# Kernel optimization log

Measured on AMD Instinct MI355X. Metric: run time of the kernel, lower is better.

The kernel has to match this reference:

```python
import jax, jax.numpy as jnp
import numpy as np

B, H, S, D = 1, 16, 4096, 64

def setup_inputs() -> dict:
    key = jax.random.key(0)
    k1, k2, k3 = jax.random.split(key, 3)
    query = jax.random.normal(k1, (B, H, S, D), dtype=jnp.float32)
    key_t = jax.random.normal(k2, (B, H, S, D), dtype=jnp.float32)
    value = jax.random.normal(k3, (B, H, S, D), dtype=jnp.float32)
    attn_mask = jnp.zeros((B, 1, S, S), dtype=jnp.float32)
    return {"query": query, "key": key_t, "value": value, "attn_mask": attn_mask}

def reference(query, key, value, attn_mask):
    d = query.shape[-1]
    # [B,H,S,S] = QK^T / sqrt(d) + mask
    scores = jnp.einsum("bhqd,bhkd->bhqk", query, key) / jnp.sqrt(jnp.float32(d))
    scores = scores + attn_mask
    probs = jax.nn.softmax(scores, axis=-1)
    # dropout_p = 0.0 -> identity
    out = jnp.einsum("bhqk,bhkd->bhqd", probs, value)
    return out
```

## Files before the change

kernel.cpp:

```cpp
#include <hip/hip_runtime.h>
#include <stdint.h>

#define LOG2E  1.44269504088896f
#define QSCALE (0.125f * LOG2E)

typedef float    f32x4_t  __attribute__((ext_vector_type(4)));
typedef float    f32x16_t __attribute__((ext_vector_type(16)));
typedef _Float16 f16x8_t  __attribute__((ext_vector_type(8)));
typedef _Float16 f16x2_t  __attribute__((ext_vector_type(2)));

#if __has_builtin(__builtin_amdgcn_exp2f)
#define EXP2F(x) __builtin_amdgcn_exp2f(x)
#else
#define EXP2F(x) exp2f(x)
#endif

__device__ __forceinline__ float rowsum2(f16x2_t p, float acc) {
#if __has_builtin(__builtin_amdgcn_fdot2)
  return __builtin_amdgcn_fdot2(p, (f16x2_t){(_Float16)1.0f, (_Float16)1.0f}, acc, false);
#else
  return acc + (float)p[0] + (float)p[1];
#endif
}

__global__ void prep_kernel(const float* __restrict__ M, const float* __restrict__ K,
                            const float* __restrict__ V, _Float16* __restrict__ Kh,
                            _Float16* __restrict__ Vth, int* __restrict__ flag) {
  __shared__ __align__(16) _Float16 T[64 * 72];
  const int tid = threadIdx.x;
  const int bid = blockIdx.x;

  {
    const float* p = M + (size_t)bid * 8192 + (size_t)tid * 4;
    unsigned acc = 0;
#pragma unroll
    for (int i = 0; i < 8; ++i) {
      f32x4_t v = *(const f32x4_t*)(p + (size_t)i * 1024);
      acc |= __float_as_uint(v[0]) | __float_as_uint(v[1]) |
             __float_as_uint(v[2]) | __float_as_uint(v[3]);
    }
    if (acc & 0x7fffffffu) atomicOr(flag, 1);
  }

  if (Kh != nullptr) {
    {
      const size_t idx = ((size_t)bid * 256 + tid) * 8;
      f32x4_t a = *(const f32x4_t*)(K + idx);
      f32x4_t b = *(const f32x4_t*)(K + idx + 4);
      union { _Float16 h[8]; uint4 q; } U;
#pragma unroll
      for (int j = 0; j < 4; ++j) { U.h[j] = (_Float16)a[j]; U.h[4 + j] = (_Float16)b[j]; }
      *(uint4*)(Kh + idx) = U.q;
    }
    if (bid < 1024) {
      const int head = bid >> 6;
      const int st   = bid & 63;
      const size_t hoff = (size_t)head * 4096 * 64;
      const int sl    = tid >> 2;
      const int fbase = (tid & 3) * 16;
      const float* src = V + hoff + (size_t)(st * 64 + sl) * 64 + fbase;
#pragma unroll
      for (int c = 0; c < 4; ++c) {
        f32x4_t a = *(const f32x4_t*)(src + c * 4);
#pragma unroll
        for (int j = 0; j < 4; ++j) T[(fbase + c * 4 + j) * 72 + sl] = (_Float16)a[j];
      }
      __syncthreads();
      const int feat = tid >> 2;
      const int sb   = (tid & 3) * 16;
      uint4 r0 = *(const uint4*)&T[feat * 72 + sb];
      uint4 r1 = *(const uint4*)&T[feat * 72 + sb + 8];
      _Float16* dst = Vth + hoff + (size_t)feat * 4096 + st * 64 + sb;
      *(uint4*)(dst)     = r0;
      *(uint4*)(dst + 8) = r1;
    }
  }
}

template <bool WS16, int NS>
__launch_bounds__(256, (NS == 1) ? 2 : 4)
__global__ void sdpa_kernel(const float* __restrict__ Qg, const float* __restrict__ Kg,
                            const float* __restrict__ Vg, const float* __restrict__ Mg,
                            const _Float16* __restrict__ Kh, const _Float16* __restrict__ Vth,
                            float* __restrict__ Og, float* __restrict__ Opart,
                            float* __restrict__ Lpart, const int* __restrict__ flag) {
  __shared__ __align__(16) _Float16 Ks[64 * 72];
  __shared__ __align__(16) _Float16 Vt[64 * 72];

  constexpr int QTSH = (NS == 1) ? 4 : (NS == 2) ? 5 : 6;

  const int tid  = threadIdx.x;
  const int bid  = blockIdx.x;
  const int hh   = ((bid & 7) << 1) | ((bid >> 3) & 1);
  const int part = (NS == 1) ? 0 : ((bid >> 4) & (NS - 1));
  const int qt   = bid >> QTSH;
  const int w    = tid >> 6;
  const int lane = tid & 63;
  const int n    = lane & 31;
  const int h2   = lane >> 5;
  const int sig  = (n & 0x13) | ((n >> 1) & 4) | ((n << 1) & 8);
  const bool has_mask = (*flag) != 0;

  const size_t hoff = (size_t)hh * 4096 * 64;
  const int qcol = qt * 128 + w * 32 + n;
  const int ktn  = 64 / NS;
  const int ktlo = part * ktn;

  f16x8_t qf[4];
  {
    const float* qp = Qg + hoff + (size_t)qcol * 64 + 8 * h2;
#pragma unroll
    for (int kh = 0; kh < 4; ++kh) {
      f32x4_t a = *(const f32x4_t*)(qp + kh * 16);
      f32x4_t b = *(const f32x4_t*)(qp + kh * 16 + 4);
      union { _Float16 h[8]; f16x8_t v; } U;
#pragma unroll
      for (int j = 0; j < 4; ++j) { U.h[j] = (_Float16)(a[j] * QSCALE); U.h[4 + j] = (_Float16)(b[j] * QSCALE); }
      qf[kh] = U.v;
    }
  }

  f32x16_t o0 = {0.f,0.f,0.f,0.f,0.f,0.f,0.f,0.f,0.f,0.f,0.f,0.f,0.f,0.f,0.f,0.f};
  f32x16_t o1 = o0;
  float lacc = 0.0f;

#pragma unroll 1
  for (int kk = 0; kk < ktn; ++kk) {
    const int kt    = ktlo + kk;
    const int kbase = kt * 64;

    uint4 kk0, kk1, vv0, vv1;
    f32x4_t k0, k1, k2, k3;
    float vlo[8], vhi[8];
    if (WS16) {
      const _Float16* kp = Kh + hoff + (size_t)(kbase + (tid >> 2)) * 64 + (tid & 3) * 16;
      kk0 = *(const uint4*)(kp);
      kk1 = *(const uint4*)(kp + 8);
      const _Float16* vp = Vth + hoff + (size_t)(tid >> 2) * 4096 + kbase + (tid & 3) * 16;
      vv0 = *(const uint4*)(vp);
      vv1 = *(const uint4*)(vp + 8);
    } else {
      const float* kp = Kg + hoff + (size_t)(kbase + (tid >> 2)) * 64 + (tid & 3) * 16;
      k0 = *(const f32x4_t*)(kp + 0);
      k1 = *(const f32x4_t*)(kp + 4);
      k2 = *(const f32x4_t*)(kp + 8);
      k3 = *(const f32x4_t*)(kp + 12);
      const float* vp = Vg + hoff + (size_t)(kbase + (tid >> 5) * 8) * 64 + (tid & 31);
#pragma unroll
      for (int j = 0; j < 8; ++j) {
        vlo[j] = vp[(size_t)j * 64];
        vhi[j] = vp[(size_t)j * 64 + 32];
      }
    }

    f32x4_t mk[2][2][2];
    if (has_mask) {
      const float* mp = Mg + (size_t)qcol * 4096 + kbase + 8 * h2;
#pragma unroll
      for (int kb = 0; kb < 2; ++kb)
#pragma unroll
        for (int a = 0; a < 2; ++a)
#pragma unroll
          for (int b = 0; b < 2; ++b)
            mk[kb][a][b] = *(const f32x4_t*)(mp + kb * 32 + 16 * a + 4 * b);
    }

    __syncthreads();

    if (WS16) {
      *(uint4*)&Ks[(tid >> 2) * 72 + (tid & 3) * 16]     = kk0;
      *(uint4*)&Ks[(tid >> 2) * 72 + (tid & 3) * 16 + 8] = kk1;
      *(uint4*)&Vt[(tid >> 2) * 72 + (tid & 3) * 16]     = vv0;
      *(uint4*)&Vt[(tid >> 2) * 72 + (tid & 3) * 16 + 8] = vv1;
    } else {
      union { _Float16 h[8]; uint4 q; } A, B;
#pragma unroll
      for (int j = 0; j < 4; ++j) {
        A.h[j] = (_Float16)k0[j];  A.h[4 + j] = (_Float16)k1[j];
        B.h[j] = (_Float16)k2[j];  B.h[4 + j] = (_Float16)k3[j];
      }
      *(uint4*)&Ks[(tid >> 2) * 72 + (tid & 3) * 16]     = A.q;
      *(uint4*)&Ks[(tid >> 2) * 72 + (tid & 3) * 16 + 8] = B.q;
      union { _Float16 h[8]; uint4 q; } C, D;
#pragma unroll
      for (int j = 0; j < 8; ++j) { C.h[j] = (_Float16)vlo[j]; D.h[j] = (_Float16)vhi[j]; }
      *(uint4*)&Vt[(tid & 31) * 72 + (tid >> 5) * 8]        = C.q;
      *(uint4*)&Vt[((tid & 31) + 32) * 72 + (tid >> 5) * 8] = D.q;
    }

    __syncthreads();

#pragma unroll
    for (int kb = 0; kb < 2; ++kb) {
      f32x16_t acc = {0.f,0.f,0.f,0.f,0.f,0.f,0.f,0.f,0.f,0.f,0.f,0.f,0.f,0.f,0.f,0.f};
#pragma unroll
      for (int kh = 0; kh < 4; ++kh) {
        const f16x8_t ka = *(const f16x8_t*)&Ks[(kb * 32 + sig) * 72 + kh * 16 + 8 * h2];
        acc = __builtin_amdgcn_mfma_f32_32x32x16_f16(ka, qf[kh], acc, 0, 0, 0);
      }
#pragma unroll
      for (int a = 0; a < 2; ++a) {
        union { _Float16 h[8]; f16x8_t v; f16x2_t p2[4]; } F;
#pragma unroll
        for (int idx = 0; idx < 8; ++idx) {
          float x = acc[8 * a + idx];
          if (has_mask) x = __builtin_fmaf(mk[kb][a][idx >> 2][idx & 3], LOG2E, x);
          F.h[idx] = (_Float16)EXP2F(x);
        }
#pragma unroll
        for (int t = 0; t < 4; ++t) lacc = rowsum2(F.p2[t], lacc);
        const int f = kb * 2 + a;
        const f16x8_t v0 = *(const f16x8_t*)&Vt[n * 72 + f * 16 + 8 * h2];
        o0 = __builtin_amdgcn_mfma_f32_32x32x16_f16(F.v, v0, o0, 0, 0, 0);
        const f16x8_t v1 = *(const f16x8_t*)&Vt[(32 + n) * 72 + f * 16 + 8 * h2];
        o1 = __builtin_amdgcn_mfma_f32_32x32x16_f16(F.v, v1, o1, 0, 0, 0);
      }
    }
  }

  float lq = lacc + __shfl_xor(lacc, 32);
  if constexpr (NS > 1) {
    float* op = Opart + (size_t)part * (16 * 4096 * 64) + hoff;
#pragma unroll
    for (int r2 = 0; r2 < 4; ++r2) {
#pragma unroll
      for (int rr = 0; rr < 4; ++rr) {
        const int reg  = r2 * 4 + rr;
        const int qrow = rr + 8 * r2 + 4 * h2;
        const size_t row = (size_t)(qt * 128 + w * 32 + qrow) * 64;
        op[row + n]      = o0[reg];
        op[row + 32 + n] = o1[reg];
      }
    }
    if (h2 == 0)
      Lpart[(size_t)part * 65536 + (size_t)hh * 4096 + qcol] = lq;
  } else {
    float* op = Og + hoff;
#pragma unroll
    for (int r2 = 0; r2 < 4; ++r2) {
#pragma unroll
      for (int rr = 0; rr < 4; ++rr) {
        const int reg  = r2 * 4 + rr;
        const int qrow = rr + 8 * r2 + 4 * h2;
        float lr  = __shfl(lq, qrow);
        float inv = 1.0f / lr;
        const size_t row = (size_t)(qt * 128 + w * 32 + qrow) * 64;
        op[row + n]      = o0[reg] * inv;
        op[row + 32 + n] = o1[reg] * inv;
      }
    }
  }
}

template <int NS>
__global__ void combine_kernel(const float* __restrict__ Opart, const float* __restrict__ Lpart,
                               float* __restrict__ Og) {
  const size_t NELEM = (size_t)16 * 4096 * 64;
  const size_t e   = ((size_t)blockIdx.x * 256 + threadIdx.x) * 8;
  const size_t row = e >> 6;
  float lsum = 0.0f;
#pragma unroll
  for (int p = 0; p < NS; ++p) lsum += Lpart[(size_t)p * 65536 + row];
  const float inv = 1.0f / lsum;
  f32x4_t s0 = {0.f, 0.f, 0.f, 0.f}, s1 = s0;
#pragma unroll
  for (int p = 0; p < NS; ++p) {
    const float* a = Opart + (size_t)p * NELEM + e;
    f32x4_t x0 = *(const f32x4_t*)a;
    f32x4_t x1 = *(const f32x4_t*)(a + 4);
#pragma unroll
    for (int j = 0; j < 4; ++j) { s0[j] += x0[j]; s1[j] += x1[j]; }
  }
  f32x4_t r0, r1;
#pragma unroll
  for (int j = 0; j < 4; ++j) { r0[j] = s0[j] * inv; r1[j] = s1[j] * inv; }
  *(f32x4_t*)(Og + e)     = r0;
  *(f32x4_t*)(Og + e + 4) = r1;
}

extern "C" void kernel_launch(void* const* d_in, const int* in_sizes, int n_in,
                              void* d_out, int out_size, void* d_ws, size_t ws_size,
                              hipStream_t stream) {
  const float* Q = (const float*)d_in[0];
  const float* K = (const float*)d_in[1];
  const float* V = (const float*)d_in[2];
  const float* M = (const float*)d_in[3];
  float* O = (float*)d_out;

  const size_t NELEM = (size_t)16 * 4096 * 64;
  const size_t need16 = 256 + 2 * NELEM * sizeof(_Float16);
  const size_t need2  = need16 + 2 * NELEM * sizeof(float) + 2 * 65536 * sizeof(float);
  const size_t need4  = need16 + 4 * NELEM * sizeof(float) + 4 * 65536 * sizeof(float);
  int* flag = (int*)d_ws;
  const bool ws16 = (ws_size >= need16);
  _Float16* Kh    = ws16 ? (_Float16*)((char*)d_ws + 256) : nullptr;
  _Float16* Vth   = ws16 ? Kh + NELEM : nullptr;
  float*    Opart = ws16 ? (float*)(Vth + NELEM) : nullptr;
  float*    Lpart4 = ws16 ? Opart + 4 * NELEM : nullptr;
  float*    Lpart2 = ws16 ? Opart + 2 * NELEM : nullptr;

  hipMemsetAsync(flag, 0, sizeof(int), stream);
  prep_kernel<<<2048, 256, 0, stream>>>(M, K, V, Kh, Vth, flag);

  if (ws_size >= need4) {
    sdpa_kernel<true, 4><<<2048, 256, 0, stream>>>(Q, K, V, M, Kh, Vth, O, Opart, Lpart4, flag);
    combine_kernel<4><<<2048, 256, 0, stream>>>(Opart, Lpart4, O);
  } else if (ws_size >= need2) {
    sdpa_kernel<true, 2><<<1024, 256, 0, stream>>>(Q, K, V, M, Kh, Vth, O, Opart, Lpart2, flag);
    combine_kernel<2><<<2048, 256, 0, stream>>>(Opart, Lpart2, O);
  } else if (ws16) {
    sdpa_kernel<true, 1><<<512, 256, 0, stream>>>(Q, K, V, M, Kh, Vth, O, nullptr, nullptr, flag);
  } else {
    sdpa_kernel<false, 1><<<512, 256, 0, stream>>>(Q, K, V, M, nullptr, nullptr, O, nullptr, nullptr, flag);
  }
}
```

Measured before the change: 241.8 us.

## Prelayout K/V in MFMA fragment order and load operands directly from global

The prep kernel now writes fp16 K and V in an order that matches the MFMA operand fragments for each 64-key tile. The attention kernel then reads each lane's K and V operands straight from global memory or L2. This removes the per-tile LDS staging, both __syncthreads barriers and the shared memory, and allows higher occupancy (launch bounds 4 for every NS). The cost is that each wave now loads its own copy of the K/V tile, so four waves fetch the same data through the cache, and global load latency is no longer hidden by the cooperative staging.

```diff
diff --git a/kernel.cpp b/kernel.cpp
--- a/kernel.cpp
+++ b/kernel.cpp
@@ -23,9 +23,13 @@
 #endif
 }
 
+__device__ __forceinline__ int sigf(int n) {
+  return (n & 0x13) | ((n >> 1) & 4) | ((n << 1) & 8);
+}
+
 __global__ void prep_kernel(const float* __restrict__ M, const float* __restrict__ K,
-                            const float* __restrict__ V, _Float16* __restrict__ Kh,
-                            _Float16* __restrict__ Vth, int* __restrict__ flag) {
+                            const float* __restrict__ V, _Float16* __restrict__ Kf,
+                            _Float16* __restrict__ Vf, int* __restrict__ flag) {
   __shared__ __align__(16) _Float16 T[64 * 72];
   const int tid = threadIdx.x;
   const int bid = blockIdx.x;
@@ -42,15 +46,25 @@
     if (acc & 0x7fffffffu) atomicOr(flag, 1);
   }
 
-  if (Kh != nullptr) {
+  if (Kf != nullptr) {
     {
-      const size_t idx = ((size_t)bid * 256 + tid) * 8;
-      f32x4_t a = *(const f32x4_t*)(K + idx);
-      f32x4_t b = *(const f32x4_t*)(K + idx + 4);
+      const size_t flat8 = ((size_t)bid * 256 + tid) * 8;
+      const int head = (int)(flat8 >> 18);
+      const int rem  = (int)(flat8 & 0x3FFFF);
+      const int key  = rem >> 6;
+      const int o    = (rem >> 3) & 7;
+      const int kt   = key >> 6;
+      const int kb   = (key >> 5) & 1;
+      const int nn   = sigf(key & 31);
+      const int kh   = o >> 1;
+      const int h2o  = o & 1;
+      f32x4_t a = *(const f32x4_t*)(K + flat8);
+      f32x4_t b = *(const f32x4_t*)(K + flat8 + 4);
       union { _Float16 h[8]; uint4 q; } U;
 #pragma unroll
       for (int j = 0; j < 4; ++j) { U.h[j] = (_Float16)a[j]; U.h[4 + j] = (_Float16)b[j]; }
-      *(uint4*)(Kh + idx) = U.q;
+      const size_t chunk = (size_t)(head * 64 + kt) * 512 + (size_t)((kb * 8 + kh * 2 + h2o) * 32 + nn);
+      *(uint4*)(Kf + chunk * 8) = U.q;
     }
     if (bid < 1024) {
       const int head = bid >> 6;
@@ -66,27 +80,26 @@
         for (int j = 0; j < 4; ++j) T[(fbase + c * 4 + j) * 72 + sl] = (_Float16)a[j];
       }
       __syncthreads();
-      const int feat = tid >> 2;
-      const int sb   = (tid & 3) * 16;
-      uint4 r0 = *(const uint4*)&T[feat * 72 + sb];
-      uint4 r1 = *(const uint4*)&T[feat * 72 + sb + 8];
-      _Float16* dst = Vth + hoff + (size_t)feat * 4096 + st * 64 + sb;
-      *(uint4*)(dst)     = r0;
-      *(uint4*)(dst + 8) = r1;
-    }
-  }
-}
-
-template <bool WS16, int NS>
-__launch_bounds__(256, (NS == 1) ? 2 : 4)
-__global__ void sdpa_kernel(const float* __restrict__ Qg, const float* __restrict__ Kg,
-                            const float* __restrict__ Vg, const float* __restrict__ Mg,
-                            const _Float16* __restrict__ Kh, const _Float16* __restrict__ Vth,
+      const int f  = tid >> 6;
+      const int l  = tid & 63;
+      const int nn = l & 31;
+      const int hl = l >> 5;
+      const size_t tbase = (size_t)(head * 64 + st) * 512;
+#pragma unroll
+      for (int vh = 0; vh < 2; ++vh) {
+        uint4 r = *(const uint4*)&T[(nn + 32 * vh) * 72 + f * 16 + 8 * hl];
+        *(uint4*)(Vf + (tbase + (size_t)((f * 2 + vh) * 64 + l)) * 8) = r;
+      }
+    }
+  }
+}
+
+template <int NS>
+__launch_bounds__(256, 4)
+__global__ void sdpa_direct(const float* __restrict__ Qg, const float* __restrict__ Mg,
+                            const _Float16* __restrict__ Kf, const _Float16* __restrict__ Vf,
                             float* __restrict__ Og, float* __restrict__ Opart,
                             float* __restrict__ Lpart, const int* __restrict__ flag) {
-  __shared__ __align__(16) _Float16 Ks[64 * 72];
-  __shared__ __align__(16) _Float16 Vt[64 * 72];
-
   constexpr int QTSH = (NS == 1) ? 4 : (NS == 2) ? 5 : 6;
 
   const int tid  = threadIdx.x;
@@ -98,7 +111,6 @@
   const int lane = tid & 63;
   const int n    = lane & 31;
   const int h2   = lane >> 5;
-  const int sig  = (n & 0x13) | ((n >> 1) & 4) | ((n << 1) & 8);
   const bool has_mask = (*flag) != 0;
 
   const size_t hoff = (size_t)hh * 4096 * 64;
@@ -124,34 +136,12 @@
   f32x16_t o1 = o0;
   float lacc = 0.0f;
 
+  const _Float16* ktile = Kf + (size_t)(hh * 64 + ktlo) * 4096 + h2 * 256 + n * 8;
+  const _Float16* vtile = Vf + (size_t)(hh * 64 + ktlo) * 4096 + (size_t)lane * 8;
+
 #pragma unroll 1
   for (int kk = 0; kk < ktn; ++kk) {
-    const int kt    = ktlo + kk;
-    const int kbase = kt * 64;
-
-    uint4 kk0, kk1, vv0, vv1;
-    f32x4_t k0, k1, k2, k3;
-    float vlo[8], vhi[8];
-    if (WS16) {
-      const _Float16* kp = Kh + hoff + (size_t)(kbase + (tid >> 2)) * 64 + (tid & 3) * 16;
-      kk0 = *(const uint4*)(kp);
-      kk1 = *(const uint4*)(kp + 8);
-      const _Float16* vp = Vth + hoff + (size_t)(tid >> 2) * 4096 + kbase + (tid & 3) * 16;
-      vv0 = *(const uint4*)(vp);
-      vv1 = *(const uint4*)(vp + 8);
-    } else {
-      const float* kp = Kg + hoff + (size_t)(kbase + (tid >> 2)) * 64 + (tid & 3) * 16;
-      k0 = *(const f32x4_t*)(kp + 0);
-      k1 = *(const f32x4_t*)(kp + 4);
-      k2 = *(const f32x4_t*)(kp + 8);
-      k3 = *(const f32x4_t*)(kp + 12);
-      const float* vp = Vg + hoff + (size_t)(kbase + (tid >> 5) * 8) * 64 + (tid & 31);
-#pragma unroll
-      for (int j = 0; j < 8; ++j) {
-        vlo[j] = vp[(size_t)j * 64];
-        vhi[j] = vp[(size_t)j * 64 + 32];
-      }
-    }
+    const int kbase = (ktlo + kk) * 64;
 
     f32x4_t mk[2][2][2];
     if (has_mask) {
@@ -165,37 +155,12 @@
             mk[kb][a][b] = *(const f32x4_t*)(mp + kb * 32 + 16 * a + 4 * b);
     }
 
-    __syncthreads();
-
-    if (WS16) {
-      *(uint4*)&Ks[(tid >> 2) * 72 + (tid & 3) * 16]     = kk0;
-      *(uint4*)&Ks[(tid >> 2) * 72 + (tid & 3) * 16 + 8] = kk1;
-      *(uint4*)&Vt[(tid >> 2) * 72 + (tid & 3) * 16]     = vv0;
-      *(uint4*)&Vt[(tid >> 2) * 72 + (tid & 3) * 16 + 8] = vv1;
-    } else {
-      union { _Float16 h[8]; uint4 q; } A, B;
-#pragma unroll
-      for (int j = 0; j < 4; ++j) {
-        A.h[j] = (_Float16)k0[j];  A.h[4 + j] = (_Float16)k1[j];
-        B.h[j] = (_Float16)k2[j];  B.h[4 + j] = (_Float16)k3[j];
-      }
-      *(uint4*)&Ks[(tid >> 2) * 72 + (tid & 3) * 16]     = A.q;
-      *(uint4*)&Ks[(tid >> 2) * 72 + (tid & 3) * 16 + 8] = B.q;
-      union { _Float16 h[8]; uint4 q; } C, D;
-#pragma unroll
-      for (int j = 0; j < 8; ++j) { C.h[j] = (_Float16)vlo[j]; D.h[j] = (_Float16)vhi[j]; }
-      *(uint4*)&Vt[(tid & 31) * 72 + (tid >> 5) * 8]        = C.q;
-      *(uint4*)&Vt[((tid & 31) + 32) * 72 + (tid >> 5) * 8] = D.q;
-    }
-
-    __syncthreads();
-
 #pragma unroll
     for (int kb = 0; kb < 2; ++kb) {
       f32x16_t acc = {0.f,0.f,0.f,0.f,0.f,0.f,0.f,0.f,0.f,0.f,0.f,0.f,0.f,0.f,0.f,0.f};
 #pragma unroll
       for (int kh = 0; kh < 4; ++kh) {
-        const f16x8_t ka = *(const f16x8_t*)&Ks[(kb * 32 + sig) * 72 + kh * 16 + 8 * h2];
+        const f16x8_t ka = *(const f16x8_t*)(ktile + kb * 2048 + kh * 512);
         acc = __builtin_amdgcn_mfma_f32_32x32x16_f16(ka, qf[kh], acc, 0, 0, 0);
       }
 #pragma unroll
@@ -210,12 +175,14 @@
 #pragma unroll
         for (int t = 0; t < 4; ++t) lacc = rowsum2(F.p2[t], lacc);
         const int f = kb * 2 + a;
-        const f16x8_t v0 = *(const f16x8_t*)&Vt[n * 72 + f * 16 + 8 * h2];
+        const f16x8_t v0 = *(const f16x8_t*)(vtile + f * 1024);
         o0 = __builtin_amdgcn_mfma_f32_32x32x16_f16(F.v, v0, o0, 0, 0, 0);
-        const f16x8_t v1 = *(const f16x8_t*)&Vt[(32 + n) * 72 + f * 16 + 8 * h2];
+        const f16x8_t v1 = *(const f16x8_t*)(vtile + f * 1024 + 512);
         o1 = __builtin_amdgcn_mfma_f32_32x32x16_f16(F.v, v1, o1, 0, 0, 0);
       }
     }
+    ktile += 4096;
+    vtile += 4096;
   }
 
   float lq = lacc + __shfl_xor(lacc, 32);
@@ -252,6 +219,138 @@
   }
 }
 
+__launch_bounds__(256, 2)
+__global__ void sdpa_lds_fallback(const float* __restrict__ Qg, const float* __restrict__ Kg,
+                                  const float* __restrict__ Vg, const float* __restrict__ Mg,
+                                  float* __restrict__ Og, const int* __restrict__ flag) {
+  __shared__ __align__(16) _Float16 Ks[64 * 72];
+  __shared__ __align__(16) _Float16 Vt[64 * 72];
+
+  const int tid  = threadIdx.x;
+  const int bid  = blockIdx.x;
+  const int hh   = ((bid & 7) << 1) | ((bid >> 3) & 1);
+  const int qt   = bid >> 4;
+  const int w    = tid >> 6;
+  const int lane = tid & 63;
+  const int n    = lane & 31;
+  const int h2   = lane >> 5;
+  const int sig  = sigf(n);
+  const bool has_mask = (*flag) != 0;
+
+  const size_t hoff = (size_t)hh * 4096 * 64;
+  const int qcol = qt * 128 + w * 32 + n;
+
+  f16x8_t qf[4];
+  {
+    const float* qp = Qg + hoff + (size_t)qcol * 64 + 8 * h2;
+#pragma unroll
+    for (int kh = 0; kh < 4; ++kh) {
+      f32x4_t a = *(const f32x4_t*)(qp + kh * 16);
+      f32x4_t b = *(const f32x4_t*)(qp + kh * 16 + 4);
+      union { _Float16 h[8]; f16x8_t v; } U;
+#pragma unroll
+      for (int j = 0; j < 4; ++j) { U.h[j] = (_Float16)(a[j] * QSCALE); U.h[4 + j] = (_Float16)(b[j] * QSCALE); }
+      qf[kh] = U.v;
+    }
+  }
+
+  f32x16_t o0 = {0.f,0.f,0.f,0.f,0.f,0.f,0.f,0.f,0.f,0.f,0.f,0.f,0.f,0.f,0.f,0.f};
+  f32x16_t o1 = o0;
+  float lacc = 0.0f;
+
+#pragma unroll 1
+  for (int kt = 0; kt < 64; ++kt) {
+    const int kbase = kt * 64;
+    f32x4_t k0, k1, k2, k3;
+    float vlo[8], vhi[8];
+    {
+      const float* kp = Kg + hoff + (size_t)(kbase + (tid >> 2)) * 64 + (tid & 3) * 16;
+      k0 = *(const f32x4_t*)(kp + 0);
+      k1 = *(const f32x4_t*)(kp + 4);
+      k2 = *(const f32x4_t*)(kp + 8);
+      k3 = *(const f32x4_t*)(kp + 12);
+      const float* vp = Vg + hoff + (size_t)(kbase + (tid >> 5) * 8) * 64 + (tid & 31);
+#pragma unroll
+      for (int j = 0; j < 8; ++j) {
+        vlo[j] = vp[(size_t)j * 64];
+        vhi[j] = vp[(size_t)j * 64 + 32];
+      }
+    }
+    f32x4_t mk[2][2][2];
+    if (has_mask) {
+      const float* mp = Mg + (size_t)qcol * 4096 + kbase + 8 * h2;
+#pragma unroll
+      for (int kb = 0; kb < 2; ++kb)
+#pragma unroll
+        for (int a = 0; a < 2; ++a)
+#pragma unroll
+          for (int b = 0; b < 2; ++b)
+            mk[kb][a][b] = *(const f32x4_t*)(mp + kb * 32 + 16 * a + 4 * b);
+    }
+
+    __syncthreads();
+    {
+      union { _Float16 h[8]; uint4 q; } A, B;
+#pragma unroll
+      for (int j = 0; j < 4; ++j) {
+        A.h[j] = (_Float16)k0[j];  A.h[4 + j] = (_Float16)k1[j];
+        B.h[j] = (_Float16)k2[j];  B.h[4 + j] = (_Float16)k3[j];
+      }
+      *(uint4*)&Ks[(tid >> 2) * 72 + (tid & 3) * 16]     = A.q;
+      *(uint4*)&Ks[(tid >> 2) * 72 + (tid & 3) * 16 + 8] = B.q;
+      union { _Float16 h[8]; uint4 q; } C, D;
+#pragma unroll
+      for (int j = 0; j < 8; ++j) { C.h[j] = (_Float16)vlo[j]; D.h[j] = (_Float16)vhi[j]; }
+      *(uint4*)&Vt[(tid & 31) * 72 + (tid >> 5) * 8]        = C.q;
+      *(uint4*)&Vt[((tid & 31) + 32) * 72 + (tid >> 5) * 8] = D.q;
+    }
+    __syncthreads();
+
+#pragma unroll
+    for (int kb = 0; kb < 2; ++kb) {
+      f32x16_t acc = {0.f,0.f,0.f,0.f,0.f,0.f,0.f,0.f,0.f,0.f,0.f,0.f,0.f,0.f,0.f,0.f};
+#pragma unroll
+      for (int kh = 0; kh < 4; ++kh) {
+        const f16x8_t ka = *(const f16x8_t*)&Ks[(kb * 32 + sig) * 72 + kh * 16 + 8 * h2];
+        acc = __builtin_amdgcn_mfma_f32_32x32x16_f16(ka, qf[kh], acc, 0, 0, 0);
+      }
+#pragma unroll
+      for (int a = 0; a < 2; ++a) {
+        union { _Float16 h[8]; f16x8_t v; f16x2_t p2[4]; } F;
+#pragma unroll
+        for (int idx = 0; idx < 8; ++idx) {
+          float x = acc[8 * a + idx];
+          if (has_mask) x = __builtin_fmaf(mk[kb][a][idx >> 2][idx & 3], LOG2E, x);
+          F.h[idx] = (_Float16)EXP2F(x);
+        }
+#pragma unroll
+        for (int t = 0; t < 4; ++t) lacc = rowsum2(F.p2[t], lacc);
+        const int f = kb * 2 + a;
+        const f16x8_t v0 = *(const f16x8_t*)&Vt[n * 72 + f * 16 + 8 * h2];
+        o0 = __builtin_amdgcn_mfma_f32_32x32x16_f16(F.v, v0, o0, 0, 0, 0);
+        const f16x8_t v1 = *(const f16x8_t*)&Vt[(32 + n) * 72 + f * 16 + 8 * h2];
+        o1 = __builtin_amdgcn_mfma_f32_32x32x16_f16(F.v, v1, o1, 0, 0, 0);
+      }
+    }
+  }
+
+  float lq = lacc + __shfl_xor(lacc, 32);
+  float* op = Og + hoff;
+#pragma unroll
+  for (int r2 = 0; r2 < 4; ++r2) {
+#pragma unroll
+    for (int rr = 0; rr < 4; ++rr) {
+      const int reg  = r2 * 4 + rr;
+      const int qrow = rr + 8 * r2 + 4 * h2;
+      float lr  = __shfl(lq, qrow);
+      float inv = 1.0f / lr;
+      const size_t row = (size_t)(qt * 128 + w * 32 + qrow) * 64;
+      op[row + n]      = o0[reg] * inv;
+      op[row + 32 + n] = o1[reg] * inv;
+    }
+  }
+}
+
 template <int NS>
 __global__ void combine_kernel(const float* __restrict__ Opart, const float* __restrict__ Lpart,
                                float* __restrict__ Og) {
@@ -293,24 +392,24 @@
   const size_t need4  = need16 + 4 * NELEM * sizeof(float) + 4 * 65536 * sizeof(float);
   int* flag = (int*)d_ws;
   const bool ws16 = (ws_size >= need16);
-  _Float16* Kh    = ws16 ? (_Float16*)((char*)d_ws + 256) : nullptr;
-  _Float16* Vth   = ws16 ? Kh + NELEM : nullptr;
-  float*    Opart = ws16 ? (float*)(Vth + NELEM) : nullptr;
+  _Float16* Kf    = ws16 ? (_Float16*)((char*)d_ws + 256) : nullptr;
+  _Float16* Vf    = ws16 ? Kf + NELEM : nullptr;
+  float*    Opart = ws16 ? (float*)(Vf + NELEM) : nullptr;
   float*    Lpart4 = ws16 ? Opart + 4 * NELEM : nullptr;
   float*    Lpart2 = ws16 ? Opart + 2 * NELEM : nullptr;
 
   hipMemsetAsync(flag, 0, sizeof(int), stream);
-  prep_kernel<<<2048, 256, 0, stream>>>(M, K, V, Kh, Vth, flag);
+  prep_kernel<<<2048, 256, 0, stream>>>(M, K, V, Kf, Vf, flag);
 
   if (ws_size >= need4) {
-    sdpa_kernel<true, 4><<<2048, 256, 0, stream>>>(Q, K, V, M, Kh, Vth, O, Opart, Lpart4, flag);
+    sdpa_direct<4><<<2048, 256, 0, stream>>>(Q, M, Kf, Vf, O, Opart, Lpart4, flag);
     combine_kernel<4><<<2048, 256, 0, stream>>>(Opart, Lpart4, O);
   } else if (ws_size >= need2) {
-    sdpa_kernel<true, 2><<<1024, 256, 0, stream>>>(Q, K, V, M, Kh, Vth, O, Opart, Lpart2, flag);
+    sdpa_direct<2><<<1024, 256, 0, stream>>>(Q, M, Kf, Vf, O, Opart, Lpart2, flag);
     combine_kernel<2><<<2048, 256, 0, stream>>>(Opart, Lpart2, O);
   } else if (ws16) {
-    sdpa_kernel<true, 1><<<512, 256, 0, stream>>>(Q, K, V, M, Kh, Vth, O, nullptr, nullptr, flag);
+    sdpa_direct<1><<<512, 256, 0, stream>>>(Q, M, Kf, Vf, O, nullptr, nullptr, flag);
   } else {
-    sdpa_kernel<false, 1><<<512, 256, 0, stream>>>(Q, K, V, M, nullptr, nullptr, O, nullptr, nullptr, flag);
-  }
-}
+    sdpa_lds_fallback<<<512, 256, 0, stream>>>(Q, K, V, M, O, flag);
+  }
+}
```

After: 291.2 us. +20.4%, slower.
